# Kernel tuning notes

Measured on AMD Instinct MI355X. Metric: run time of the kernel, lower is better.

Reference implementation:

```python
import jax, jax.numpy as jnp
import numpy as np

L, D, H, DFF, V = 6, 1024, 16, 4096, 32000
B, S_SRC, S_TGT = 4, 512, 512
DK = D // H
NEG = -1.0e9


def _ln(x, g, b, eps=1e-5):
    mu = jnp.mean(x, axis=-1, keepdims=True)
    var = jnp.mean((x - mu) ** 2, axis=-1, keepdims=True)
    return (x - mu) / jnp.sqrt(var + eps) * g + b


def _rope_tables(seq_len, dk):
    inv_freq = 1.0 / (10000.0 ** (jnp.arange(0, dk, 2, dtype=jnp.float32) / dk))
    ang = jnp.arange(seq_len, dtype=jnp.float32)[:, None] * inv_freq[None, :]  # [S, dk/2]
    return jnp.cos(ang), jnp.sin(ang)


def _apply_rope(x, cos, sin):
    # x: [B, H, S, dk]; interleaved-pair rotation
    x1, x2 = x[..., 0::2], x[..., 1::2]
    r1 = x1 * cos - x2 * sin
    r2 = x1 * sin + x2 * cos
    return jnp.stack([r1, r2], axis=-1).reshape(x.shape)


def _mha(q_in, kv_in, Wq, bq, Wk, bk, Wv, bv, Wo, bo, mask, cs_q, cs_k):
    Bq, Sq, _ = q_in.shape
    Sk = kv_in.shape[1]
    Q = (q_in @ Wq + bq).reshape(Bq, Sq, H, DK).transpose(0, 2, 1, 3)
    K = (kv_in @ Wk + bk).reshape(Bq, Sk, H, DK).transpose(0, 2, 1, 3)
    Vv = (kv_in @ Wv + bv).reshape(Bq, Sk, H, DK).transpose(0, 2, 1, 3)
    Q = _apply_rope(Q, *cs_q)
    K = _apply_rope(K, *cs_k)
    scores = jnp.einsum('bhqd,bhkd->bhqk', Q, K) / jnp.sqrt(jnp.float32(DK))
    scores = jnp.where(mask, scores, NEG)
    probs = jax.nn.softmax(scores, axis=-1)
    out = jnp.einsum('bhqk,bhkd->bhqd', probs, Vv)
    out = out.transpose(0, 2, 1, 3).reshape(Bq, Sq, D)
    return out @ Wo + bo


def setup_inputs() -> dict:
    key = jax.random.key(0)
    ks = iter(jax.random.split(key, 64))
    w = lambda *sh: (jax.random.normal(next(ks), sh, dtype=jnp.float32) * 0.02)
    inp = {}
    inp['src'] = jax.random.randint(next(ks), (B, S_SRC), 0, V)
    inp['tgt'] = jax.random.randint(next(ks), (B, S_TGT), 0, V)
    # embeddings with padding_idx=1 zeroed (TokenEmbedding2)
    inp['enc_emb'] = w(V, D).at[1].set(0.0)
    inp['dec_emb'] = w(V, D).at[1].set(0.0)
    for p in ['eWq', 'eWk', 'eWv', 'eWo']:
        inp[p] = w(L, D, D)
    for p in ['eBq', 'eBk', 'eBv', 'eBo']:
        inp[p] = jnp.zeros((L, D), jnp.float32)
    inp['eL1g'] = jnp.ones((L, D), jnp.float32); inp['eL1b'] = jnp.zeros((L, D), jnp.float32)
    inp['eL2g'] = jnp.ones((L, D), jnp.float32); inp['eL2b'] = jnp.zeros((L, D), jnp.float32)
    inp['eF1'] = w(L, D, DFF); inp['eF1b'] = jnp.zeros((L, DFF), jnp.float32)
    inp['eF2'] = w(L, DFF, D); inp['eF2b'] = jnp.zeros((L, D), jnp.float32)
    for p in ['dsWq', 'dsWk', 'dsWv', 'dsWo', 'dcWq', 'dcWk', 'dcWv', 'dcWo']:
        inp[p] = w(L, D, D)
    for p in ['dsBq', 'dsBk', 'dsBv', 'dsBo', 'dcBq', 'dcBk', 'dcBv', 'dcBo']:
        inp[p] = jnp.zeros((L, D), jnp.float32)
    for p in ['dL1g', 'dL2g', 'dL3g']:
        inp[p] = jnp.ones((L, D), jnp.float32)
    for p in ['dL1b', 'dL2b', 'dL3b']:
        inp[p] = jnp.zeros((L, D), jnp.float32)
    inp['dF1'] = w(L, D, DFF); inp['dF1b'] = jnp.zeros((L, DFF), jnp.float32)
    inp['dF2'] = w(L, DFF, D); inp['dF2b'] = jnp.zeros((L, D), jnp.float32)
    inp['fW'] = w(D, V); inp['fb'] = jnp.zeros((V,), jnp.float32)
    return inp


def reference(src, tgt, enc_emb, dec_emb,
              eWq, eBq, eWk, eBk, eWv, eBv, eWo, eBo,
              eL1g, eL1b, eL2g, eL2b, eF1, eF1b, eF2, eF2b,
              dsWq, dsBq, dsWk, dsBk, dsWv, dsBv, dsWo, dsBo,
              dcWq, dcBq, dcWk, dcBk, dcWv, dcBv, dcWo, dcBo,
              dL1g, dL1b, dL2g, dL2b, dL3g, dL3b,
              dF1, dF1b, dF2, dF2b, fW, fb):
    # masks, per Transformer.create_masks (pad token id == 0)
    src_mask = (src != 0)[:, None, None, :]                                   # [B,1,1,Ss]
    causal = jnp.tril(jnp.ones((S_TGT, S_TGT), bool))                          # [T,T]
    tgt_mask = (tgt != 0)[:, None, None, :] & causal[None, None]               # [B,1,T,T]

    cs_src = _rope_tables(S_SRC, DK)
    cs_tgt = _rope_tables(S_TGT, DK)

    # encoder (dropout is identity in eval)
    x = enc_emb[src]
    for l in range(L):
        a = _mha(x, x, eWq[l], eBq[l], eWk[l], eBk[l], eWv[l], eBv[l],
                 eWo[l], eBo[l], src_mask, cs_src, cs_src)
        x = _ln(x + a, eL1g[l], eL1b[l])
        f = jax.nn.relu(x @ eF1[l] + eF1b[l]) @ eF2[l] + eF2b[l]
        x = _ln(x + f, eL2g[l], eL2b[l])
    memory = x

    # decoder
    y = dec_emb[tgt]
    for l in range(L):
        a = _mha(y, y, dsWq[l], dsBq[l], dsWk[l], dsBk[l], dsWv[l], dsBv[l],
                 dsWo[l], dsBo[l], tgt_mask, cs_tgt, cs_tgt)
        y = _ln(y + a, dL1g[l], dL1b[l])
        a = _mha(y, memory, dcWq[l], dcBq[l], dcWk[l], dcBk[l], dcWv[l], dcBv[l],
                 dcWo[l], dcBo[l], src_mask, cs_tgt, cs_src)
        y = _ln(y + a, dL2g[l], dL2b[l])
        f = jax.nn.relu(y @ dF1[l] + dF1b[l]) @ dF2[l] + dF2b[l]
        y = _ln(y + f, dL3g[l], dL3b[l])

    logits = y @ fW + fb
    return jax.nn.softmax(logits, axis=-1)
```

## Files before the change

### kernel.cpp

```cpp
#include <hip/hip_runtime.h>
#include <math.h>

#define NLAYER 6
#define DMODEL 1024
#define NHEAD  16
#define DFFN   4096
#define VOCAB  32000
#define NBATCH 4
#define SEQLEN 512
#define HDIM   64
#define MROWS  (NBATCH*SEQLEN)
#define MiB    (1024L*1024L)

typedef __attribute__((ext_vector_type(8))) short bf16x8;
typedef __attribute__((ext_vector_type(4))) float f32x4;
typedef unsigned short u16;

__device__ __forceinline__ float waveSum(float v) {
#pragma unroll
  for (int off = 32; off > 0; off >>= 1) v += __shfl_xor(v, off);
  return v;
}
__device__ __forceinline__ u16 f2bf(float x) {
  unsigned u = __float_as_uint(x);
  u += 0x7FFFu + ((u >> 16) & 1u);
  return (u16)(u >> 16);
}
__device__ __forceinline__ float bf2f(u16 h) {
  return __uint_as_float((unsigned)h << 16);
}
__device__ __forceinline__ void load_lds16(const u16* src, u16* dst) {
  __builtin_amdgcn_global_load_lds(
      (const __attribute__((address_space(1))) unsigned int*)src,
      (__attribute__((address_space(3))) unsigned int*)dst, 16, 0, 0);
}


__global__ __launch_bounds__(256) void embed_t_kernel(
    const int* __restrict__ tok, const float* __restrict__ emb,
    float* __restrict__ out, u16* __restrict__ th)
{
  const long row = blockIdx.x;
  const int t = tok[row];
  const int k0 = threadIdx.x * 4;
  const float4 v = *(const float4*)(emb + (long)t * DMODEL + k0);
  *(float4*)(out + row * DMODEL + k0) = v;
  const long off = ((row >> 4) * 32 + (k0 >> 5)) * 512 +
                   (long)(((k0 & 31) >> 3)) * 128 + (row & 15) * 8 + (k0 & 7);
  uint2 uh;
  uh.x = (unsigned)f2bf(v.x) | ((unsigned)f2bf(v.y) << 16);
  uh.y = (unsigned)f2bf(v.z) | ((unsigned)f2bf(v.w) << 16);
  *(uint2*)(th + off) = uh;
}

__global__ __launch_bounds__(256) void rope_tab_kernel(float* __restrict__ cosT, float* __restrict__ sinT)
{
  const int idx = blockIdx.x * 256 + threadIdx.x;
  const int s = idx >> 5, i = idx & 31;
  const float e = (float)(2 * i) / 64.0f;
  const float inv = 1.0f / powf(10000.0f, e);
  const float ang = (float)s * inv;
  cosT[idx] = cosf(ang);
  sinT[idx] = sinf(ang);
}

__global__ __launch_bounds__(256) void wconv_kernel(
    const float* __restrict__ W, u16* __restrict__ Wh,
    int K, int ldN, int nbase)
{
  __shared__ float tile[32][68];
  const int t = threadIdx.x;
  const int k0 = blockIdx.x * 32, n0 = blockIdx.y * 64;
  {
    const int r = t >> 3, c = (t & 7) * 8;
    const float* wp = W + (long)(k0 + r) * ldN + nbase + n0 + c;
    *(float4*)&tile[r][c]     = *(const float4*)wp;
    *(float4*)&tile[r][c + 4] = *(const float4*)(wp + 4);
  }
  __syncthreads();
  const int fr = t & 15, kg = (t >> 4) & 3, nb = t >> 6;
  const int n = nb * 16 + fr;
  unsigned ph[4];
#pragma unroll
  for (int i = 0; i < 4; ++i) {
    const float x0 = tile[kg * 8 + 2 * i][n];
    const float x1 = tile[kg * 8 + 2 * i + 1][n];
    ph[i] = (unsigned)f2bf(x0) | ((unsigned)f2bf(x1) << 16);
  }
  const int tk = K >> 5;
  const long off = ((long)(n0 / 16 + nb) * tk + (k0 >> 5)) * 512 + kg * 128 + fr * 8;
  *(uint4*)(Wh + off) = make_uint4(ph[0], ph[1], ph[2], ph[3]);
}

__global__ __launch_bounds__(256) void wconv_ffn_kernel(
    const float* __restrict__ W1, const float* __restrict__ W2,
    u16* __restrict__ f1h, u16* __restrict__ f2h)
{
  __shared__ float tile[32][68];
  const int bx = blockIdx.x, t = threadIdx.x;
  const float* W; u16* out; int K, ldN, k0, n0;
  if (bx < 2048) { W = W1; out = f1h; K = 1024; ldN = 4096; k0 = (bx & 31) * 32;  n0 = (bx >> 5) * 64; }
  else { const int xx = bx - 2048; W = W2; out = f2h; K = 4096; ldN = 1024; k0 = (xx & 127) * 32; n0 = (xx >> 7) * 64; }
  {
    const int r = t >> 3, c = (t & 7) * 8;
    const float* wp = W + (long)(k0 + r) * ldN + n0 + c;
    *(float4*)&tile[r][c]     = *(const float4*)wp;
    *(float4*)&tile[r][c + 4] = *(const float4*)(wp + 4);
  }
  __syncthreads();
  const int fr = t & 15, kg = (t >> 4) & 3, nb = t >> 6;
  const int n = nb * 16 + fr;
  unsigned ph[4];
#pragma unroll
  for (int i = 0; i < 4; ++i) {
    const float x0 = tile[kg * 8 + 2 * i][n];
    const float x1 = tile[kg * 8 + 2 * i + 1][n];
    ph[i] = (unsigned)f2bf(x0) | ((unsigned)f2bf(x1) << 16);
  }
  const int tk = K >> 5;
  const long off = ((long)(n0 / 16 + nb) * tk + (k0 >> 5)) * 512 + kg * 128 + fr * 8;
  *(uint4*)(out + off) = make_uint4(ph[0], ph[1], ph[2], ph[3]);
}

__global__ __launch_bounds__(256) void wconv_attn_kernel(
    const float* __restrict__ Wq, const float* __restrict__ Wk,
    const float* __restrict__ Wv, const float* __restrict__ Wo,
    const float* __restrict__ Bq, const float* __restrict__ Bk,
    const float* __restrict__ Bv,
    u16* __restrict__ aWh, u16* __restrict__ oWh, float* __restrict__ fusedB)
{
  __shared__ float tile[32][68];
  const int zz = blockIdx.z;
  const float* W = (zz == 0) ? Wq : (zz == 1) ? Wk : (zz == 2) ? Wv : Wo;
  u16* Wh = (zz < 3) ? aWh : oWh;
  const int obase = (zz < 3) ? zz * 1024 : 0;
  const int t = threadIdx.x;
  const int k0 = blockIdx.x * 32, n0 = blockIdx.y * 64;
  if (zz < 3 && blockIdx.x == 0 && blockIdx.y < 4) {
    const float* B = (zz == 0) ? Bq : (zz == 1) ? Bk : Bv;
    fusedB[zz * 1024 + blockIdx.y * 256 + t] = B[blockIdx.y * 256 + t];
  }
  {
    const int r = t >> 3, c = (t & 7) * 8;
    const float* wp = W + (long)(k0 + r) * 1024 + n0 + c;
    *(float4*)&tile[r][c]     = *(const float4*)wp;
    *(float4*)&tile[r][c + 4] = *(const float4*)(wp + 4);
  }
  __syncthreads();
  const int fr = t & 15, kg = (t >> 4) & 3, nb = t >> 6;
  const int n = nb * 16 + fr;
  unsigned ph[4];
#pragma unroll
  for (int i = 0; i < 4; ++i) {
    const float x0 = tile[kg * 8 + 2 * i][n];
    const float x1 = tile[kg * 8 + 2 * i + 1][n];
    ph[i] = (unsigned)f2bf(x0) | ((unsigned)f2bf(x1) << 16);
  }
  const long off = ((long)((obase + n0) / 16 + nb) * 32 + (k0 >> 5)) * 512 + kg * 128 + fr * 8;
  *(uint4*)(Wh + off) = make_uint4(ph[0], ph[1], ph[2], ph[3]);
}

template<int BM, int BN, int OUTMODE, int CH>
__global__ __launch_bounds__(256) void gemm_t_kernel(
    const u16* __restrict__ Ah, const u16* __restrict__ Bh,
    const float* __restrict__ bias, float* __restrict__ C,
    u16* __restrict__ th, float* __restrict__ partial,
    u16* __restrict__ qkvT, const float* __restrict__ cosT,
    const float* __restrict__ sinT,
    int K, int tkA, int tkB, long ldc, int tkC, int colBase)
{
  constexpr int TA = BM / 16;
  constexpr int TB = BN / 16;
  constexpr int MREP = BM / 32;
  constexpr int NREP = BN / 32;
  constexpr int NTILES2 = (TA + TB) * CH;
  constexpr int NL2 = NTILES2 / 4;
  __shared__ __align__(16) u16 lds[NTILES2 * 512];
  const int tid = threadIdx.x, wid = tid >> 6, lane = tid & 63;
  const int fr = lane & 15, kg = lane >> 4;
  const int wr = wid >> 1, wc = wid & 1;
  const int row0 = blockIdx.x * BM, col0 = blockIdx.y * BN;
  const long aTile0 = (long)(row0 >> 4) * tkA;
  const long bTile0 = (long)(col0 >> 4) * tkB;
  const int laneOff = lane * 8;

  const u16* srcs[NL2];
  u16* dsts[NL2];
#pragma unroll
  for (int i = 0; i < NL2; ++i) {
    const int t2 = wid + i * 4;
    const int t = t2 / CH, c = t2 % CH;
    const u16* s;
    if (t < TA) s = Ah + (aTile0 + (long)t * tkA) * 512;
    else        s = Bh + (bTile0 + (long)(t - TA) * tkB) * 512;
    srcs[i] = s + c * 512 + laneOff;
    dsts[i] = lds + t2 * 512;
  }

  f32x4 acc[MREP][NREP];
#pragma unroll
  for (int m = 0; m < MREP; ++m)
#pragma unroll
    for (int n = 0; n < NREP; ++n) acc[m][n] = {0.f, 0.f, 0.f, 0.f};

  const int fo = (kg * 16 + fr) * 8;
  const u16* sA_ = lds;
  const u16* sB_ = lds + TA * CH * 512;

  for (int kc = 0; kc < K / (32 * CH); ++kc) {
#pragma unroll
    for (int i = 0; i < NL2; ++i) {
      load_lds16(srcs[i], dsts[i]);
      srcs[i] += CH * 512;
    }
    __syncthreads();
#pragma unroll
    for (int c = 0; c < CH; ++c) {
      bf16x8 fah[MREP], fbh[NREP];
#pragma unroll
      for (int m = 0; m < MREP; ++m)
        fah[m] = *(const bf16x8*)(sA_ + ((wr * MREP + m) * CH + c) * 512 + fo);
#pragma unroll
      for (int n = 0; n < NREP; ++n)
        fbh[n] = *(const bf16x8*)(sB_ + ((wc * NREP + n) * CH + c) * 512 + fo);
#pragma unroll
      for (int m = 0; m < MREP; ++m)
#pragma unroll
        for (int n = 0; n < NREP; ++n)
          acc[m][n] = __builtin_amdgcn_mfma_f32_16x16x32_bf16(fah[m], fbh[n], acc[m][n], 0, 0, 0);
    }
    __syncthreads();
  }
  if constexpr (OUTMODE == 3) {
#pragma unroll
    for (int n = 0; n < NREP; ++n) {
      const int col = col0 + (wc * NREP + n) * 16 + fr;
      const float bv = bias[col];
      const int k3 = (col >> 3) & 3;
      const int k7 = col & 7;
#pragma unroll
      for (int m = 0; m < MREP; ++m)
#pragma unroll
        for (int r = 0; r < 4; ++r) {
          const int row = row0 + (wr * MREP + m) * 16 + kg * 4 + r;
          const float v = fmaxf(acc[m][n][r] + bv, 0.f);
          const long off = ((long)(row >> 4) * tkC + (col >> 5)) * 512 + k3 * 128 + (row & 15) * 8 + k7;
          th[off] = f2bf(v);
        }
    }
  } else if constexpr (OUTMODE == 4) {
    __shared__ float rsum[BM];
    for (int i = tid; i < BM; i += 256) rsum[i] = 0.f;
    __syncthreads();
    float rs[MREP][4];
#pragma unroll
    for (int m = 0; m < MREP; ++m)
#pragma unroll
      for (int r = 0; r < 4; ++r) rs[m][r] = 0.f;
#pragma unroll
    for (int n = 0; n < NREP; ++n) {
      const int col = col0 + (wc * NREP + n) * 16 + fr;
      const float bv = bias[col];
#pragma unroll
      for (int m = 0; m < MREP; ++m)
#pragma unroll
        for (int r = 0; r < 4; ++r) {
          const long row = row0 + (wr * MREP + m) * 16 + kg * 4 + r;
          const float e = __expf(acc[m][n][r] + bv);
          C[row * ldc + col] = e;
          rs[m][r] += e;
        }
    }
#pragma unroll
    for (int m = 0; m < MREP; ++m)
#pragma unroll
      for (int r = 0; r < 4; ++r) {
#pragma unroll
        for (int off = 1; off < 16; off <<= 1) rs[m][r] += __shfl_xor(rs[m][r], off, 16);
        if (fr == 0) atomicAdd(&rsum[(wr * MREP + m) * 16 + kg * 4 + r], rs[m][r]);
      }
    __syncthreads();
    for (int i = tid; i < BM; i += 256)
      partial[(long)(row0 + i) * 256 + blockIdx.y] = rsum[i];
  } else if constexpr (OUTMODE == 5) {
    const int gc0 = colBase + col0;
    const int sect = gc0 >> 10;
    u16* T = qkvT + (long)sect * 2097152;
#pragma unroll
    for (int n = 0; n < NREP; ++n) {
      const int gcol = gc0 + (wc * NREP + n) * 16 + fr;
      const float bv = bias[gcol];
      const int hc = (gcol & 1023) >> 6;
      const int d = gcol & 63;
#pragma unroll
      for (int m = 0; m < MREP; ++m)
#pragma unroll
        for (int r = 0; r < 4; ++r) {
          const int row = row0 + (wr * MREP + m) * 16 + kg * 4 + r;
          const int b = row >> 9, s = row & 511;
          const float v = acc[m][n][r] + bv;
          const long zb = (long)(b * 16 + hc) * 32768;
          if (sect < 2) {
            const float vp = __shfl_xor(v, 1);
            const int i2 = d >> 1;
            const float cc = cosT[s * 32 + i2], ss = sinT[s * 32 + i2];
            float ro = (d & 1) ? (vp * ss + v * cc) : (v * cc - vp * ss);
            if (sect == 0) ro *= 0.125f;
            const long off = zb + ((long)(s >> 4) * 2 + (d >> 5)) * 512 +
                             ((d >> 3) & 3) * 128 + (s & 15) * 8 + (d & 7);
            T[off] = f2bf(ro);
          } else {
            const long off = zb + ((long)(d >> 4) * 16 + (s >> 5)) * 512 +
                             ((s >> 3) & 3) * 128 + (d & 15) * 8 + (s & 7);
            T[off] = f2bf(v);
          }
        }
    }
  } else {
#pragma unroll
    for (int n = 0; n < NREP; ++n) {
      const int col = col0 + (wc * NREP + n) * 16 + fr;
      const float bv = bias ? bias[col] : 0.f;
#pragma unroll
      for (int m = 0; m < MREP; ++m)
#pragma unroll
        for (int r = 0; r < 4; ++r) {
          const long row = row0 + (wr * MREP + m) * 16 + kg * 4 + r;
          C[row * ldc + col] = acc[m][n][r] + bv;
        }
    }
  }
}

__global__ __launch_bounds__(256) void flash_kernel(
    const u16* __restrict__ Qt, const u16* __restrict__ Kt,
    const u16* __restrict__ Vt, const int* __restrict__ tok,
    u16* __restrict__ Oh, int causal)
{
  __shared__ __align__(16) u16 sKV[16 * 512];
  __shared__ __align__(16) u16 sP[8 * 512];
  const int tid = threadIdx.x, wid = tid >> 6, lane = tid & 63;
  const int fr = lane & 15, kg = lane >> 4;
  const int qblk = blockIdx.x, z = blockIdx.y;
  const int b = z >> 4, h = z & 15;
  const long zbase = (long)z * 32768;
  const int fo = (kg * 16 + fr) * 8;
  const int laneOff = lane * 8;
  int kblim = 8;
  if (causal && tok[b * 512] != 0) kblim = qblk + 1;
  bf16x8 qf[2];
#pragma unroll
  for (int kc = 0; kc < 2; ++kc)
    qf[kc] = *(const bf16x8*)(Qt + zbase + ((long)(qblk * 4 + wid) * 2 + kc) * 512 + fo);
  f32x4 acc_o[4];
  float lp[4];
#pragma unroll
  for (int n = 0; n < 4; ++n) acc_o[n] = {0.f, 0.f, 0.f, 0.f};
#pragma unroll
  for (int r = 0; r < 4; ++r) lp[r] = 0.f;

  for (int kb = 0; kb < kblim; ++kb) {
    __syncthreads();
#pragma unroll
    for (int i = 0; i < 4; ++i) {
      const int t = wid + i * 4;
      const u16* src;
      if (t < 8) src = Kt + zbase + (long)((kb * 4 + (t >> 1)) * 2 + (t & 1)) * 512;
      else       src = Vt + zbase + (long)(((t - 8) >> 1) * 16 + kb * 2 + (t & 1)) * 512;
      load_lds16(src + laneOff, sKV + t * 512);
    }
    __syncthreads();
    f32x4 s4[4];
#pragma unroll
    for (int n = 0; n < 4; ++n) s4[n] = {0.f, 0.f, 0.f, 0.f};
#pragma unroll
    for (int kc = 0; kc < 2; ++kc)
#pragma unroll
      for (int n = 0; n < 4; ++n) {
        const bf16x8 kf = *(const bf16x8*)(sKV + (n * 2 + kc) * 512 + fo);
        s4[n] = __builtin_amdgcn_mfma_f32_16x16x32_bf16(qf[kc], kf, s4[n], 0, 0, 0);
      }
    int tmask[4];
#pragma unroll
    for (int n = 0; n < 4; ++n) tmask[n] = tok[b * 512 + kb * 64 + n * 16 + fr];
#pragma unroll
    for (int r = 0; r < 4; ++r) {
      const int q = qblk * 64 + wid * 16 + kg * 4 + r;
#pragma unroll
      for (int n = 0; n < 4; ++n) {
        const int kcol = kb * 64 + n * 16 + fr;
        const bool ok = (tmask[n] != 0) && (!causal || kcol <= q);
        const float p = __expf(ok ? s4[n][r] : -30.0f);
        lp[r] += p;
        const int k3 = (n & 1) * 2 + (fr >> 3);
        sP[(wid * 2 + (n >> 1)) * 512 + k3 * 128 + (kg * 4 + r) * 8 + (fr & 7)] = f2bf(p);
      }
    }
    __syncthreads();
#pragma unroll
    for (int kc = 0; kc < 2; ++kc) {
      const bf16x8 pf = *(const bf16x8*)(sP + (wid * 2 + kc) * 512 + fo);
#pragma unroll
      for (int n = 0; n < 4; ++n) {
        const bf16x8 vf = *(const bf16x8*)(sKV + (8 + n * 2 + kc) * 512 + fo);
        acc_o[n] = __builtin_amdgcn_mfma_f32_16x16x32_bf16(pf, vf, acc_o[n], 0, 0, 0);
      }
    }
  }
#pragma unroll
  for (int r = 0; r < 4; ++r) {
    float s = lp[r];
#pragma unroll
    for (int off = 1; off < 16; off <<= 1) s += __shfl_xor(s, off, 16);
    const float inv = 1.0f / s;
#pragma unroll
    for (int n = 0; n < 4; ++n) acc_o[n][r] *= inv;
  }
  __syncthreads();
#pragma unroll
  for (int n = 0; n < 4; ++n)
#pragma unroll
    for (int r = 0; r < 4; ++r) {
      const int k3 = (n & 1) * 2 + (fr >> 3);
      sP[(wid * 2 + (n >> 1)) * 512 + k3 * 128 + (kg * 4 + r) * 8 + (fr & 7)] = f2bf(acc_o[n][r]);
    }
  __syncthreads();
  const long rbg = (long)b * 32 + qblk * 4 + wid;
#pragma unroll
  for (int i = 0; i < 2; ++i) {
    const long off = (rbg * 32 + h * 2 + i) * 512 + laneOff;
    *(uint4*)(Oh + off) = *(const uint4*)(sP + (wid * 2 + i) * 512 + laneOff);
  }
}

__global__ __launch_bounds__(256) void ln_fused_kernel(
    const float* __restrict__ X, const float* __restrict__ R,
    const float* __restrict__ g, const float* __restrict__ be,
    float* __restrict__ Out, u16* __restrict__ th)
{
  __shared__ float red[8];
  const int tid = threadIdx.x;
  const long row = blockIdx.x;
  const int k0 = tid * 4;
  const float4 xv = *(const float4*)(X + row * DMODEL + k0);
  const float4 rv = *(const float4*)(R + row * DMODEL + k0);
  const float v0 = xv.x + rv.x, v1 = xv.y + rv.y, v2 = xv.z + rv.z, v3 = xv.w + rv.w;
  float s = waveSum((v0 + v1) + (v2 + v3));
  const int wv = tid >> 6, ln = tid & 63;
  if (ln == 0) red[wv] = s;
  __syncthreads();
  const float mu = (red[0] + red[1] + red[2] + red[3]) * (1.0f / DMODEL);
  const float d0 = v0 - mu, d1 = v1 - mu, d2 = v2 - mu, d3 = v3 - mu;
  float sq = waveSum(d0 * d0 + d1 * d1 + d2 * d2 + d3 * d3);
  if (ln == 0) red[4 + wv] = sq;
  __syncthreads();
  const float var = (red[4] + red[5] + red[6] + red[7]) * (1.0f / DMODEL);
  const float rstd = 1.0f / sqrtf(var + 1e-5f);
  const float4 gv = *(const float4*)(g + k0);
  const float4 bv = *(const float4*)(be + k0);
  float4 o;
  o.x = d0 * rstd * gv.x + bv.x;
  o.y = d1 * rstd * gv.y + bv.y;
  o.z = d2 * rstd * gv.z + bv.z;
  o.w = d3 * rstd * gv.w + bv.w;
  *(float4*)(Out + row * DMODEL + k0) = o;
  const long off = ((row >> 4) * 32 + (k0 >> 5)) * 512 +
                   (long)(((k0 & 31) >> 3)) * 128 + (row & 15) * 8 + (k0 & 7);
  uint2 uh;
  uh.x = (unsigned)f2bf(o.x) | ((unsigned)f2bf(o.y) << 16);
  uh.y = (unsigned)f2bf(o.z) | ((unsigned)f2bf(o.w) << 16);
  *(uint2*)(th + off) = uh;
}

__global__ __launch_bounds__(256) void vocab_norm_kernel(
    float* __restrict__ P, const float* __restrict__ partial)
{
  __shared__ float red[4];
  const int tid = threadIdx.x;
  const long row = blockIdx.x;
  float s = (tid < 250) ? partial[row * 256 + tid] : 0.f;
  s = waveSum(s);
  const int wv = tid >> 6, ln = tid & 63;
  if (ln == 0) red[wv] = s;
  __syncthreads();
  const float inv = 1.0f / (red[0] + red[1] + red[2] + red[3]);
  float4* p = (float4*)(P + row * VOCAB);
  for (int i = tid; i < VOCAB / 4; i += 256) {
    float4 v = p[i];
    v.x *= inv; v.y *= inv; v.z *= inv; v.w *= inv;
    p[i] = v;
  }
}

extern "C" void kernel_launch(void* const* d_in, const int* in_sizes, int n_in,
                              void* d_out, int out_size, void* d_ws, size_t ws_size,
                              hipStream_t stream)
{
  (void)in_sizes; (void)n_in; (void)out_size; (void)ws_size;
  const int* src = (const int*)d_in[0];
  const int* tgt = (const int*)d_in[1];
  const float* enc_emb = (const float*)d_in[2];
  const float* dec_emb = (const float*)d_in[3];
  const float* eWq = (const float*)d_in[4];
  const float* eWk = (const float*)d_in[5];
  const float* eWv = (const float*)d_in[6];
  const float* eWo = (const float*)d_in[7];
  const float* eBq = (const float*)d_in[8];
  const float* eBk = (const float*)d_in[9];
  const float* eBv = (const float*)d_in[10];
  const float* eBo = (const float*)d_in[11];
  const float* eL1g = (const float*)d_in[12];
  const float* eL1b = (const float*)d_in[13];
  const float* eL2g = (const float*)d_in[14];
  const float* eL2b = (const float*)d_in[15];
  const float* eF1  = (const float*)d_in[16];
  const float* eF1b = (const float*)d_in[17];
  const float* eF2  = (const float*)d_in[18];
  const float* eF2b = (const float*)d_in[19];
  const float* dsWq = (const float*)d_in[20];
  const float* dsWk = (const float*)d_in[21];
  const float* dsWv = (const float*)d_in[22];
  const float* dsWo = (const float*)d_in[23];
  const float* dcWq = (const float*)d_in[24];
  const float* dcWk = (const float*)d_in[25];
  const float* dcWv = (const float*)d_in[26];
  const float* dcWo = (const float*)d_in[27];
  const float* dsBq = (const float*)d_in[28];
  const float* dsBk = (const float*)d_in[29];
  const float* dsBv = (const float*)d_in[30];
  const float* dsBo = (const float*)d_in[31];
  const float* dcBq = (const float*)d_in[32];
  const float* dcBk = (const float*)d_in[33];
  const float* dcBv = (const float*)d_in[34];
  const float* dcBo = (const float*)d_in[35];
  const float* dL1g = (const float*)d_in[36];
  const float* dL2g = (const float*)d_in[37];
  const float* dL3g = (const float*)d_in[38];
  const float* dL1b = (const float*)d_in[39];
  const float* dL2b = (const float*)d_in[40];
  const float* dL3b = (const float*)d_in[41];
  const float* dF1  = (const float*)d_in[42];
  const float* dF1b = (const float*)d_in[43];
  const float* dF2  = (const float*)d_in[44];
  const float* dF2b = (const float*)d_in[45];
  const float* fW   = (const float*)d_in[46];
  const float* fb   = (const float*)d_in[47];

  char* base = (char*)d_ws;
  auto alloc = [&](size_t bytes) { char* p = base; base += (bytes + 1023) & ~(size_t)1023; return p; };
  float* cosT   = (float*)alloc(SEQLEN * 32 * 4);
  float* sinT   = (float*)alloc(SEQLEN * 32 * 4);
  float* fusedB = (float*)alloc(3072 * 4);
  float* xb  = (float*)alloc((long)MROWS * DMODEL * 4);
  float* yb  = (float*)alloc((long)MROWS * DMODEL * 4);
  float* pb  = (float*)alloc((long)MROWS * DMODEL * 4);
  u16*   mt  = (u16*)alloc((long)MROWS * DMODEL * 2);
  char* rA = base;
  u16* sth  = (u16*)(rA + 0 * MiB);
  u16* aWh  = (u16*)(rA + 8 * MiB);
  u16* qkvT = (u16*)(rA + 14 * MiB);
  u16* ath  = (u16*)(rA + 26 * MiB);
  u16* oWh  = (u16*)(rA + 30 * MiB);
  u16* f1h = (u16*)(rA + 8 * MiB);
  u16* f2h = (u16*)(rA + 16 * MiB);
  u16* fth = (u16*)(rA + 24 * MiB);
  u16* vh  = (u16*)(rA + 8 * MiB);
  float* vpart = (float*)(rA + 71 * MiB);
  u16* Qt = qkvT;
  u16* Kt = qkvT + 2097152;
  u16* Vt = qkvT + 2 * 2097152;

  const long DD = (long)DMODEL * DMODEL;
  const long DF = (long)DMODEL * DFFN;

  rope_tab_kernel<<<(SEQLEN * 32) / 256, 256, 0, stream>>>(cosT, sinT);

  auto attention = [&](int self, const float* Wq, const float* Bq,
                       const float* Wk, const float* Bk,
                       const float* Wv, const float* Bv,
                       const float* Wo, const float* Bo,
                       const int* tok, int causal) {
    wconv_attn_kernel<<<dim3(32, 16, 4), 256, 0, stream>>>(
        Wq, Wk, Wv, Wo, Bq, Bk, Bv, aWh, oWh, fusedB);
    if (self) {
      gemm_t_kernel<128, 64, 5, 2><<<dim3(16, 48), 256, 0, stream>>>(
          sth, aWh, fusedB, nullptr, nullptr, nullptr, qkvT, cosT, sinT,
          1024, 32, 32, 0, 0, 0);
    } else {
      gemm_t_kernel<64, 64, 5, 2><<<dim3(32, 16), 256, 0, stream>>>(
          sth, aWh, fusedB, nullptr, nullptr, nullptr, qkvT, cosT, sinT,
          1024, 32, 32, 0, 0, 0);
      gemm_t_kernel<128, 64, 5, 2><<<dim3(16, 32), 256, 0, stream>>>(
          mt, aWh + (long)64 * 32 * 512, fusedB, nullptr, nullptr, nullptr, qkvT, cosT, sinT,
          1024, 32, 32, 0, 0, 1024);
    }
    flash_kernel<<<dim3(8, 64), 256, 0, stream>>>(Qt, Kt, Vt, tok, ath, causal);
    gemm_t_kernel<64, 64, 0, 2><<<dim3(32, 16), 256, 0, stream>>>(
        ath, oWh, Bo, pb, nullptr, nullptr, nullptr, nullptr, nullptr,
        1024, 32, 32, 1024, 0, 0);
  };

  auto ffn = [&](const float* W1, const float* B1, const float* W2, const float* B2) {
    wconv_ffn_kernel<<<4096, 256, 0, stream>>>(W1, W2, f1h, f2h);
    gemm_t_kernel<128, 64, 3, 2><<<dim3(16, 64), 256, 0, stream>>>(
        sth, f1h, B1, nullptr, fth, nullptr, nullptr, nullptr, nullptr,
        1024, 32, 32, 0, 128, 0);
    gemm_t_kernel<64, 64, 0, 2><<<dim3(32, 16), 256, 0, stream>>>(
        fth, f2h, B2, pb, nullptr, nullptr, nullptr, nullptr, nullptr,
        4096, 128, 128, 1024, 0, 0);
  };

  embed_t_kernel<<<MROWS, 256, 0, stream>>>(src, enc_emb, xb, sth);
  for (int l = 0; l < NLAYER; ++l) {
    attention(1, eWq + l * DD, eBq + l * DMODEL, eWk + l * DD, eBk + l * DMODEL,
              eWv + l * DD, eBv + l * DMODEL, eWo + l * DD, eBo + l * DMODEL, src, 0);
    ln_fused_kernel<<<MROWS, 256, 0, stream>>>(xb, pb, eL1g + l * DMODEL, eL1b + l * DMODEL,
                                               xb, sth);
    ffn(eF1 + l * DF, eF1b + l * DFFN, eF2 + l * DF, eF2b + l * DMODEL);
    ln_fused_kernel<<<MROWS, 256, 0, stream>>>(xb, pb, eL2g + l * DMODEL, eL2b + l * DMODEL,
                                               xb, (l == NLAYER - 1) ? mt : sth);
  }
  embed_t_kernel<<<MROWS, 256, 0, stream>>>(tgt, dec_emb, yb, sth);
  for (int l = 0; l < NLAYER; ++l) {
    attention(1, dsWq + l * DD, dsBq + l * DMODEL, dsWk + l * DD, dsBk + l * DMODEL,
              dsWv + l * DD, dsBv + l * DMODEL, dsWo + l * DD, dsBo + l * DMODEL, tgt, 1);
    ln_fused_kernel<<<MROWS, 256, 0, stream>>>(yb, pb, dL1g + l * DMODEL, dL1b + l * DMODEL,
                                               yb, sth);
    attention(0, dcWq + l * DD, dcBq + l * DMODEL, dcWk + l * DD, dcBk + l * DMODEL,
              dcWv + l * DD, dcBv + l * DMODEL, dcWo + l * DD, dcBo + l * DMODEL, src, 0);
    ln_fused_kernel<<<MROWS, 256, 0, stream>>>(yb, pb, dL2g + l * DMODEL, dL2b + l * DMODEL,
                                               yb, sth);
    ffn(dF1 + l * DF, dF1b + l * DFFN, dF2 + l * DF, dF2b + l * DMODEL);
    ln_fused_kernel<<<MROWS, 256, 0, stream>>>(yb, pb, dL3g + l * DMODEL, dL3b + l * DMODEL,
                                               yb, sth);
  }
  float* outp = (float*)d_out;
  wconv_kernel<<<dim3(32, 500), 256, 0, stream>>>(fW, vh, 1024, VOCAB, 0);
  gemm_t_kernel<128, 128, 4, 1><<<dim3(16, 250), 256, 0, stream>>>(
      sth, vh, fb, outp, nullptr, vpart, nullptr, nullptr, nullptr,
      1024, 32, 32, VOCAB, 0, 0);
  vocab_norm_kernel<<<MROWS, 256, 0, stream>>>(outp, vpart);
}
```

Baseline: 2.871 ms.

## Process 128-key tiles in flash attention, add MFMA priority hints, retune GEMM params

```diff
diff --git a/kernel.cpp b/kernel.cpp
--- a/kernel.cpp
+++ b/kernel.cpp
@@ -337,8 +337,8 @@
     const u16* __restrict__ Vt, const int* __restrict__ tok,
     u16* __restrict__ Oh, int causal)
 {
-  __shared__ __align__(16) u16 sKV[16 * 512];
-  __shared__ __align__(16) u16 sP[8 * 512];
+  __shared__ __align__(16) u16 sKV[32 * 512];
+  __shared__ __align__(16) u16 sP[16 * 512];
   const int tid = threadIdx.x, wid = tid >> 6, lane = tid & 63;
   const int fr = lane & 15, kg = lane >> 4;
   const int qblk = blockIdx.x, z = blockIdx.y;
@@ -346,8 +346,8 @@
   const long zbase = (long)z * 32768;
   const int fo = (kg * 16 + fr) * 8;
   const int laneOff = lane * 8;
-  int kblim = 8;
-  if (causal && tok[b * 512] != 0) kblim = qblk + 1;
+  int kb2lim = 4;
+  if (causal && tok[b * 512] != 0) kb2lim = (qblk + 2) >> 1;
   bf16x8 qf[2];
 #pragma unroll
   for (int kc = 0; kc < 2; ++kc)
@@ -359,53 +359,61 @@
 #pragma unroll
   for (int r = 0; r < 4; ++r) lp[r] = 0.f;
 
-  for (int kb = 0; kb < kblim; ++kb) {
+  for (int kb2 = 0; kb2 < kb2lim; ++kb2) {
     __syncthreads();
 #pragma unroll
-    for (int i = 0; i < 4; ++i) {
+    for (int i = 0; i < 8; ++i) {
       const int t = wid + i * 4;
       const u16* src;
-      if (t < 8) src = Kt + zbase + (long)((kb * 4 + (t >> 1)) * 2 + (t & 1)) * 512;
-      else       src = Vt + zbase + (long)(((t - 8) >> 1) * 16 + kb * 2 + (t & 1)) * 512;
+      if (t < 16) {
+        src = Kt + zbase + (long)((kb2 * 8 + (t >> 1)) * 2 + (t & 1)) * 512;
+      } else {
+        const int u = t - 16;
+        src = Vt + zbase + (long)((u >> 2) * 16 + kb2 * 4 + (u & 3)) * 512;
+      }
       load_lds16(src + laneOff, sKV + t * 512);
     }
     __syncthreads();
-    f32x4 s4[4];
-#pragma unroll
-    for (int n = 0; n < 4; ++n) s4[n] = {0.f, 0.f, 0.f, 0.f};
+    f32x4 s4[8];
+#pragma unroll
+    for (int n = 0; n < 8; ++n) s4[n] = {0.f, 0.f, 0.f, 0.f};
+    __builtin_amdgcn_s_setprio(1);
 #pragma unroll
     for (int kc = 0; kc < 2; ++kc)
 #pragma unroll
-      for (int n = 0; n < 4; ++n) {
+      for (int n = 0; n < 8; ++n) {
         const bf16x8 kf = *(const bf16x8*)(sKV + (n * 2 + kc) * 512 + fo);
         s4[n] = __builtin_amdgcn_mfma_f32_16x16x32_bf16(qf[kc], kf, s4[n], 0, 0, 0);
       }
-    int tmask[4];
-#pragma unroll
-    for (int n = 0; n < 4; ++n) tmask[n] = tok[b * 512 + kb * 64 + n * 16 + fr];
+    __builtin_amdgcn_s_setprio(0);
+    int tmask[8];
+#pragma unroll
+    for (int n = 0; n < 8; ++n) tmask[n] = tok[b * 512 + kb2 * 128 + n * 16 + fr];
 #pragma unroll
     for (int r = 0; r < 4; ++r) {
       const int q = qblk * 64 + wid * 16 + kg * 4 + r;
 #pragma unroll
-      for (int n = 0; n < 4; ++n) {
-        const int kcol = kb * 64 + n * 16 + fr;
+      for (int n = 0; n < 8; ++n) {
+        const int kcol = kb2 * 128 + n * 16 + fr;
         const bool ok = (tmask[n] != 0) && (!causal || kcol <= q);
         const float p = __expf(ok ? s4[n][r] : -30.0f);
         lp[r] += p;
-        const int k3 = (n & 1) * 2 + (fr >> 3);
-        sP[(wid * 2 + (n >> 1)) * 512 + k3 * 128 + (kg * 4 + r) * 8 + (fr & 7)] = f2bf(p);
+        sP[(wid * 4 + (n >> 1)) * 512 + ((n & 1) * 2 + (fr >> 3)) * 128 +
+           (kg * 4 + r) * 8 + (fr & 7)] = f2bf(p);
       }
     }
     __syncthreads();
-#pragma unroll
-    for (int kc = 0; kc < 2; ++kc) {
-      const bf16x8 pf = *(const bf16x8*)(sP + (wid * 2 + kc) * 512 + fo);
+    __builtin_amdgcn_s_setprio(1);
+#pragma unroll
+    for (int kc2 = 0; kc2 < 4; ++kc2) {
+      const bf16x8 pf = *(const bf16x8*)(sP + (wid * 4 + kc2) * 512 + fo);
 #pragma unroll
       for (int n = 0; n < 4; ++n) {
-        const bf16x8 vf = *(const bf16x8*)(sKV + (8 + n * 2 + kc) * 512 + fo);
+        const bf16x8 vf = *(const bf16x8*)(sKV + (16 + n * 4 + kc2) * 512 + fo);
         acc_o[n] = __builtin_amdgcn_mfma_f32_16x16x32_bf16(pf, vf, acc_o[n], 0, 0, 0);
       }
     }
+    __builtin_amdgcn_s_setprio(0);
   }
 #pragma unroll
   for (int r = 0; r < 4; ++r) {
@@ -605,7 +613,7 @@
     gemm_t_kernel<128, 64, 3, 2><<<dim3(16, 64), 256, 0, stream>>>(
         sth, f1h, B1, nullptr, fth, nullptr, nullptr, nullptr, nullptr,
         1024, 32, 32, 0, 128, 0);
-    gemm_t_kernel<64, 64, 0, 2><<<dim3(32, 16), 256, 0, stream>>>(
+    gemm_t_kernel<64, 64, 0, 4><<<dim3(32, 16), 256, 0, stream>>>(
         fth, f2h, B2, pb, nullptr, nullptr, nullptr, nullptr, nullptr,
         4096, 128, 128, 1024, 0, 0);
   };
@@ -636,7 +644,7 @@
   }
   float* outp = (float*)d_out;
   wconv_kernel<<<dim3(32, 500), 256, 0, stream>>>(fW, vh, 1024, VOCAB, 0);
-  gemm_t_kernel<128, 128, 4, 1><<<dim3(16, 250), 256, 0, stream>>>(
+  gemm_t_kernel<128, 128, 4, 2><<<dim3(16, 250), 256, 0, stream>>>(
       sth, vh, fb, outp, nullptr, vpart, nullptr, nullptr, nullptr,
       1024, 32, 32, VOCAB, 0, 0);
   vocab_norm_kernel<<<MROWS, 256, 0, stream>>>(outp, vpart);
```

New measurement: 2.716 ms. 1.06x faster.
